# Performance work log

Hardware: AMD Instinct MI355X
Metric: run time of the kernel (lower is better)

The kernel has to match this reference:

```python
import jax, jax.numpy as jnp
import numpy as np

N, E, CIN, COUT = 50000, 800000, 64, 64
K_MAIN, K_SC = 5, 1
EPS = 1e-15      # PyG GMMConv sigma epsilon
BN_EPS = 1e-5    # BatchNorm epsilon


def gmm_conv(x, src, dst, pseudo, g, mu, sigma, root, bias):
    """PyG GMMConv with aggr='mean', root_weight=True, bias=True.
    x: [N,Cin], pseudo: [E,dim], g: [Cin,K*Cout], mu/sigma: [K,dim],
    root: [Cin,Cout], bias: [Cout]."""
    K = mu.shape[0]
    Cout = root.shape[1]
    n = x.shape[0]
    # Gaussian mixture weights per edge: [E,K]
    diff = pseudo[:, None, :] - mu[None, :, :]                     # [E,K,dim]
    gauss = jnp.exp((-0.5 * diff * diff / (EPS + sigma[None] ** 2)).sum(-1))
    # Project node features once at node level, then gather per edge
    xp = (x @ g).reshape(n, K, Cout)                               # [N,K,Cout]
    msg = jnp.einsum('ek,ekc->ec', gauss, xp[src])                 # [E,Cout]
    agg = jax.ops.segment_sum(msg, dst, num_segments=n)            # [N,Cout]
    deg = jax.ops.segment_sum(jnp.ones((src.shape[0],), x.dtype), dst,
                              num_segments=n)
    agg = agg / jnp.clip(deg, 1.0)[:, None]                        # mean aggr
    return agg + x @ root + bias


def batch_norm(x, gamma, beta):
    # SyncBatchNorm in training mode: batch stats over the node dimension
    m = x.mean(0)
    v = x.var(0)  # biased variance, as torch uses for normalization
    return (x - m) * jax.lax.rsqrt(v + BN_EPS) * gamma + beta


def _gmm_params(key, cin, cout, k):
    k1, k2, k3, k4 = jax.random.split(key, 4)
    scale = 1.0 / np.sqrt(cin)
    g = jax.random.normal(k1, (cin, k * cout), jnp.float32) * scale
    mu = jax.random.uniform(k2, (k, 1), jnp.float32)
    sigma = 1.0 + 0.1 * jax.random.uniform(k3, (k, 1), jnp.float32)
    root = jax.random.normal(k4, (cin, cout), jnp.float32) * scale
    bias = jnp.zeros((cout,), jnp.float32)
    return g, mu, sigma, root, bias


def setup_inputs() -> dict:
    key = jax.random.key(0)
    ks = jax.random.split(key, 8)
    x = jax.random.normal(ks[0], (N, CIN), jnp.float32)
    edge_index = jax.random.randint(ks[1], (2, E), 0, N, jnp.int64)
    edge_attr = jax.random.uniform(ks[2], (E, 1), jnp.float32)
    g1, mu1, sig1, root1, b1 = _gmm_params(ks[3], CIN, COUT, K_MAIN)
    g2, mu2, sig2, root2, b2 = _gmm_params(ks[4], COUT, COUT, K_MAIN)
    gs, mus, sigs, roots, bs = _gmm_params(ks[5], CIN, COUT, K_SC)
    ones = jnp.ones((COUT,), jnp.float32)
    zeros = jnp.zeros((COUT,), jnp.float32)
    return {
        'x': x, 'edge_index': edge_index, 'edge_attr': edge_attr,
        'g1': g1, 'mu1': mu1, 'sig1': sig1, 'root1': root1, 'b1': b1,
        'gam1': ones, 'bet1': zeros,
        'g2': g2, 'mu2': mu2, 'sig2': sig2, 'root2': root2, 'b2': b2,
        'gam2': ones, 'bet2': zeros,
        'gs': gs, 'mus': mus, 'sigs': sigs, 'roots': roots, 'bs': bs,
        'gams': ones, 'bets': zeros,
    }


def reference(x, edge_index, edge_attr,
              g1, mu1, sig1, root1, b1, gam1, bet1,
              g2, mu2, sig2, root2, b2, gam2, bet2,
              gs, mus, sigs, roots, bs, gams, bets):
    src, dst = edge_index[0], edge_index[1]
    h = gmm_conv(x, src, dst, edge_attr, g1, mu1, sig1, root1, b1)
    h = jax.nn.elu(batch_norm(h, gam1, bet1))
    h = gmm_conv(h, src, dst, edge_attr, g2, mu2, sig2, root2, b2)
    h = batch_norm(h, gam2, bet2)
    sc = gmm_conv(x, src, dst, edge_attr, gs, mus, sigs, roots, bs)
    sc = batch_norm(sc, gams, bets)
    return jax.nn.elu(h + sc)
```

## Files before the change

### kernel.cpp

```cpp
#include <hip/hip_runtime.h>
#include <hip/hip_bf16.h>


#define EPS_SIGMA 1e-15f
#define BN_EPS    1e-5f

typedef unsigned short ushortT;
typedef unsigned int uintT;
typedef __attribute__((ext_vector_type(8))) short bf16x8;
typedef __attribute__((ext_vector_type(4))) float f32x4;
typedef __attribute__((ext_vector_type(2))) float f32x2;

__device__ __forceinline__ ushortT f2bf(float f) {
  uintT b = __float_as_uint(f);
  b += 0x7FFFu + ((b >> 16) & 1u);
  return (ushortT)(b >> 16);
}
__device__ __forceinline__ float bf2f(ushortT u) {
  return __uint_as_float(((uintT)u) << 16);
}
__device__ __forceinline__ uintT pk2(float a, float b) {
  return (uintT)f2bf(a) | ((uintT)f2bf(b) << 16);
}

__global__ void prologue(const float* __restrict__ x, ushortT* __restrict__ x_bf,
                         int total, int* __restrict__ cnt, float* __restrict__ stats,
                         int n, const void* ei, int* flag) {
  int t = blockIdx.x * 256 + threadIdx.x;
  int idx = t * 4;
  if (idx + 3 < total) {
    float4 v = *(const float4*)&x[idx];
    ushortT o[4] = {f2bf(v.x), f2bf(v.y), f2bf(v.z), f2bf(v.w)};
    *(uint2*)&x_bf[idx] = *(const uint2*)o;
  }
  if (t < n) cnt[t] = 0;
  if (t < 12 * 64) stats[t] = 0.f;
  if (blockIdx.x == 0) {
    const int* p = (const int*)ei;
    __shared__ int bad;
    if (threadIdx.x == 0) bad = 0;
    __syncthreads();
    if (p[threadIdx.x * 2 + 1] != 0) atomicAdd(&bad, 1);
    __syncthreads();
    if (threadIdx.x == 0) *flag = (bad == 0);
  }
}

__device__ __forceinline__ int load_idx(const void* ei, size_t pos, int is64) {
  if (is64) return (int)((const long long*)ei)[pos];
  return ((const int*)ei)[pos];
}

__global__ void hist_kernel(const void* ei, int E, const int* flag, int* cnt,
                            int* __restrict__ pos) {
  int e = blockIdx.x * blockDim.x + threadIdx.x;
  if (e >= E) return;
  int d = load_idx(ei, (size_t)E + e, *flag);
  pos[e] = atomicAdd(&cnt[d], 1);
}

__global__ __launch_bounds__(256) void scan1(const int* __restrict__ cnt,
                                             int* __restrict__ row_ptr,
                                             int* __restrict__ partials, int n) {
  int tid = threadIdx.x;
  int base = blockIdx.x * 2048 + tid * 8;
  int v[8], pre[8];
  int run = 0;
#pragma unroll
  for (int j = 0; j < 8; ++j) {
    int idx = base + j;
    v[j] = (idx < n) ? cnt[idx] : 0;
    pre[j] = run;
    run += v[j];
  }
  __shared__ int sd[256];
  sd[tid] = run;
  __syncthreads();
  for (int off = 1; off < 256; off <<= 1) {
    int t = (tid >= off) ? sd[tid - off] : 0;
    __syncthreads();
    sd[tid] += t;
    __syncthreads();
  }
  int excl = sd[tid] - run;
#pragma unroll
  for (int j = 0; j < 8; ++j) {
    int idx = base + j;
    if (idx < n) row_ptr[idx] = excl + pre[j];
  }
  if (tid == 255) partials[blockIdx.x] = sd[255];
}

__global__ void scan2(int* partials, int nb, int* row_ptr, int n) {
  __shared__ int sd[256];
  int tid = threadIdx.x;
  int v = (tid < nb) ? partials[tid] : 0;
  sd[tid] = v;
  __syncthreads();
  for (int off = 1; off < 256; off <<= 1) {
    int t = (tid >= off) ? sd[tid - off] : 0;
    __syncthreads();
    sd[tid] += t;
    __syncthreads();
  }
  if (tid < nb) partials[tid] = sd[tid] - v;
  if (tid == nb - 1) row_ptr[n] = sd[tid];
}

__global__ void scan3(int* __restrict__ row_ptr, const int* __restrict__ partials, int n) {
  int i = blockIdx.x * 256 + threadIdx.x;
  if (i < n) row_ptr[i] += partials[i >> 11];
}

__global__ __launch_bounds__(256) void scatter_wgt(
    const void* ei, const float* __restrict__ ea, int E, const int* flag,
    const int* __restrict__ row_ptr, const int* __restrict__ pos,
    const float* __restrict__ mu1, const float* __restrict__ sig1,
    const float* __restrict__ mus, const float* __restrict__ sigs,
    const float* __restrict__ mu2, const float* __restrict__ sig2,
    uint4* __restrict__ wbuf1, uint4* __restrict__ wbuf2) {
  int e = blockIdx.x * 256 + threadIdx.x;
  if (e >= E) return;
  int is64 = *flag;
  int s = load_idx(ei, (size_t)e, is64);
  int d = load_idx(ei, (size_t)E + e, is64);
  int slot = row_ptr[d] + pos[e];
  float p = ea[e];
  float w1[6], w2[5];
#pragma unroll
  for (int k = 0; k < 5; ++k) {
    float sg = sig1[k], df = p - mu1[k];
    w1[k] = __expf(-0.5f / (EPS_SIGMA + sg * sg) * df * df);
  }
  {
    float sg = sigs[0], df = p - mus[0];
    w1[5] = __expf(-0.5f / (EPS_SIGMA + sg * sg) * df * df);
  }
#pragma unroll
  for (int k = 0; k < 5; ++k) {
    float sg = sig2[k], df = p - mu2[k];
    w2[k] = __expf(-0.5f / (EPS_SIGMA + sg * sg) * df * df);
  }
  wbuf1[slot] = make_uint4(pk2(w1[0], w1[1]), pk2(w1[2], w1[3]), pk2(w1[4], w1[5]), (uintT)s);
  wbuf2[slot] = make_uint4(pk2(w2[0], w2[1]), pk2(w2[2], w2[3]), pk2(w2[4], 0.f), (uintT)s);
}

template <int KT>
__device__ __forceinline__ void q_fma(f32x2* acc, uint4 r, uint2 xv) {
  f32x2 xlo, xhi;
  xlo.x = bf2f((ushortT)(xv.x & 0xffffu));
  xlo.y = bf2f((ushortT)(xv.x >> 16));
  xhi.x = bf2f((ushortT)(xv.y & 0xffffu));
  xhi.y = bf2f((ushortT)(xv.y >> 16));
  float w;
  f32x2 wv;
  w = bf2f((ushortT)(r.x & 0xffffu));
  wv.x = w; wv.y = w;
  acc[0] = __builtin_elementwise_fma(wv, xlo, acc[0]);
  acc[1] = __builtin_elementwise_fma(wv, xhi, acc[1]);
  if (KT > 1) {
    w = bf2f((ushortT)(r.x >> 16));
    wv.x = w; wv.y = w;
    acc[2] = __builtin_elementwise_fma(wv, xlo, acc[2]);
    acc[3] = __builtin_elementwise_fma(wv, xhi, acc[3]);
  }
  if (KT > 2) {
    w = bf2f((ushortT)(r.y & 0xffffu));
    wv.x = w; wv.y = w;
    acc[4] = __builtin_elementwise_fma(wv, xlo, acc[4]);
    acc[5] = __builtin_elementwise_fma(wv, xhi, acc[5]);
  }
  if (KT > 3) {
    w = bf2f((ushortT)(r.y >> 16));
    wv.x = w; wv.y = w;
    acc[6] = __builtin_elementwise_fma(wv, xlo, acc[6]);
    acc[7] = __builtin_elementwise_fma(wv, xhi, acc[7]);
  }
  if (KT > 4) {
    w = bf2f((ushortT)(r.z & 0xffffu));
    wv.x = w; wv.y = w;
    acc[8] = __builtin_elementwise_fma(wv, xlo, acc[8]);
    acc[9] = __builtin_elementwise_fma(wv, xhi, acc[9]);
  }
  if (KT > 5) {
    w = bf2f((ushortT)(r.z >> 16));
    wv.x = w; wv.y = w;
    acc[10] = __builtin_elementwise_fma(wv, xlo, acc[10]);
    acc[11] = __builtin_elementwise_fma(wv, xhi, acc[11]);
  }
}

template <int KT>
__global__ __launch_bounds__(256) void agg_pre(const ushortT* __restrict__ feat,
                                               const int* __restrict__ row_ptr,
                                               const uint4* __restrict__ wbuf,
                                               ushortT* __restrict__ out, int n, int ldo) {
  int node = blockIdx.x * 4 + (threadIdx.x >> 6);
  int lane = threadIdx.x & 63;
  int q = lane >> 4;
  int c4 = lane & 15;
  if (node >= n) return;
  int beg = row_ptr[node], end = row_ptr[node + 1];
  f32x2 acc[2 * KT];
#pragma unroll
  for (int k = 0; k < 2 * KT; ++k) acc[k] = (f32x2){0.f, 0.f};
  int i = beg;
  for (; i + 8 <= end; i += 8) {
    uint4 r0 = wbuf[i + q];
    uint4 r1 = wbuf[i + 4 + q];
    uint2 x0 = *(const uint2*)&feat[((size_t)r0.w << 6) + c4 * 4];
    uint2 x1 = *(const uint2*)&feat[((size_t)r1.w << 6) + c4 * 4];
    q_fma<KT>(acc, r0, x0);
    q_fma<KT>(acc, r1, x1);
  }
  for (; i + 4 <= end; i += 4) {
    uint4 r = wbuf[i + q];
    uint2 xv = *(const uint2*)&feat[((size_t)r.w << 6) + c4 * 4];
    q_fma<KT>(acc, r, xv);
  }
  int rem = end - i;
  if (q < rem) {
    uint4 r = wbuf[i + q];
    uint2 xv = *(const uint2*)&feat[((size_t)r.w << 6) + c4 * 4];
    q_fma<KT>(acc, r, xv);
  }
#pragma unroll
  for (int k = 0; k < 2 * KT; ++k) {
    acc[k].x += __shfl_xor(acc[k].x, 16);
    acc[k].y += __shfl_xor(acc[k].y, 16);
    acc[k].x += __shfl_xor(acc[k].x, 32);
    acc[k].y += __shfl_xor(acc[k].y, 32);
  }
  int degi = end - beg;
  float invdeg = 1.0f / (float)(degi > 1 ? degi : 1);
  if (lane < 16) {
    uintT* outu = (uintT*)out;
    size_t obase = ((size_t)node * ldo) >> 1;
#pragma unroll
    for (int k = 0; k < KT; ++k) {
      uint2 ov = make_uint2(pk2(acc[2 * k].x * invdeg, acc[2 * k].y * invdeg),
                            pk2(acc[2 * k + 1].x * invdeg, acc[2 * k + 1].y * invdeg));
      *(uint2*)&outu[obase + k * 32 + c4 * 2] = ov;
    }
  }
}

__device__ __forceinline__ void prep_one(const float* __restrict__ g,
                                         const float* __restrict__ root,
                                         ushortT* __restrict__ Bm, int K, int t) {
  int ks = t >> 8, rem = t & 255;
  int nt = rem >> 6, lane = rem & 63;
  int kbase = ks * 32 + (lane >> 4) * 8;
  int col = nt * 16 + (lane & 15);
  ushortT o[8];
#pragma unroll
  for (int j = 0; j < 8; ++j) {
    int r = kbase + j;
    float v;
    if (r < K * 64) {
      int k = r >> 6, i = r & 63;
      v = g[(size_t)i * (K * 64) + k * 64 + col];
    } else {
      v = root[(size_t)(r - K * 64) * 64 + col];
    }
    o[j] = f2bf(v);
  }
  *(uint4*)&Bm[(size_t)t * 8] = *(const uint4*)o;
}

__global__ void prep_all(const float* g1, const float* root1, ushortT* Bm1,
                         const float* g2, const float* root2, ushortT* Bm2,
                         const float* gs, const float* roots, ushortT* Bmsc) {
  int t = blockIdx.x * 256 + threadIdx.x;
  if (t < 12 * 256) prep_one(g1, root1, Bm1, 5, t);
  else if (t < 24 * 256) prep_one(g2, root2, Bm2, 5, t - 12 * 256);
  else if (t < 28 * 256) prep_one(gs, roots, Bmsc, 1, t - 24 * 256);
}

__device__ __forceinline__ void bn_epilogue(float cs[4], float cq[4], int wid, int lane,
                                            int tid, float red_s[4][64], float red_q[4][64],
                                            float* sums, float* sumsq) {
#pragma unroll
  for (int nt = 0; nt < 4; ++nt) {
    cs[nt] += __shfl_xor(cs[nt], 16);
    cs[nt] += __shfl_xor(cs[nt], 32);
    cq[nt] += __shfl_xor(cq[nt], 16);
    cq[nt] += __shfl_xor(cq[nt], 32);
  }
  if (lane < 16) {
#pragma unroll
    for (int nt = 0; nt < 4; ++nt) {
      red_s[wid][nt * 16 + lane] = cs[nt];
      red_q[wid][nt * 16 + lane] = cq[nt];
    }
  }
  __syncthreads();
  if (tid < 64) {
    float ts = red_s[0][tid] + red_s[1][tid] + red_s[2][tid] + red_s[3][tid];
    float tq = red_q[0][tid] + red_q[1][tid] + red_q[2][tid] + red_q[3][tid];
    atomicAdd(&sums[tid], ts);
    atomicAdd(&sumsq[tid], tq);
  }
  __syncthreads();
}

__global__ __launch_bounds__(256) void gemm_mfma(const ushortT* __restrict__ A1, int lda1,
                                                 int K1, const ushortT* __restrict__ A2,
                                                 const ushortT* __restrict__ Bm,
                                                 const float* __restrict__ bias,
                                                 ushortT* __restrict__ C, int M,
                                                 float* sums, float* sumsq) {
  __shared__ float red_s[4][64];
  __shared__ float red_q[4][64];
  int tid = threadIdx.x;
  int wid = tid >> 6, lane = tid & 63;
  int row16 = lane & 15, kg = lane >> 4;
  int rowbase = blockIdx.x * 64 + wid * 16;
  int arow = rowbase + row16;
  if (arow >= M) arow = M - 1;
  const ushortT* a1p = A1 + (size_t)arow * lda1 + kg * 8;
  const ushortT* a2p = A2 + (size_t)arow * 64 + kg * 8;
  int nks1 = K1 >> 5;
  int nks = (K1 + 64) >> 5;
  f32x4 acc[4];
#pragma unroll
  for (int nt = 0; nt < 4; ++nt) acc[nt] = (f32x4){0.f, 0.f, 0.f, 0.f};
  for (int ks = 0; ks < nks; ++ks) {
    const ushortT* ap = (ks < nks1) ? (a1p + ks * 32) : (a2p + (ks - nks1) * 32);
    bf16x8 af = *(const bf16x8*)ap;
#pragma unroll
    for (int nt = 0; nt < 4; ++nt) {
      bf16x8 bfr = *(const bf16x8*)(Bm + (size_t)ks * 2048 + nt * 512 + lane * 8);
      acc[nt] = __builtin_amdgcn_mfma_f32_16x16x32_bf16(af, bfr, acc[nt], 0, 0, 0);
    }
  }
  float bv[4];
#pragma unroll
  for (int nt = 0; nt < 4; ++nt) bv[nt] = bias[nt * 16 + row16];
  float cs[4] = {}, cq[4] = {};
#pragma unroll
  for (int r = 0; r < 4; ++r) {
    int orow = rowbase + kg * 4 + r;
    if (orow < M) {
#pragma unroll
      for (int nt = 0; nt < 4; ++nt) {
        float v = acc[nt][r] + bv[nt];
        C[(size_t)orow * 64 + nt * 16 + row16] = f2bf(v);
        cs[nt] += v;
        cq[nt] = fmaf(v, v, cq[nt]);
      }
    }
  }
  bn_epilogue(cs, cq, wid, lane, tid, red_s, red_q, sums, sumsq);
}

__global__ __launch_bounds__(256) void gemm_mfma_dual(
    const ushortT* __restrict__ Abuf, const ushortT* __restrict__ X,
    const ushortT* __restrict__ Bm1, const ushortT* __restrict__ Bmsc,
    const float* __restrict__ b1, const float* __restrict__ bs,
    ushortT* __restrict__ H, ushortT* __restrict__ S, int M,
    float* sumH, float* sqH, float* sumS, float* sqS) {
  __shared__ float red_s[4][64];
  __shared__ float red_q[4][64];
  int tid = threadIdx.x;
  int wid = tid >> 6, lane = tid & 63;
  int row16 = lane & 15, kg = lane >> 4;
  int rowbase = blockIdx.x * 64 + wid * 16;
  int arow = rowbase + row16;
  if (arow >= M) arow = M - 1;
  const ushortT* ab = Abuf + (size_t)arow * 384 + kg * 8;
  const ushortT* xb = X + (size_t)arow * 64 + kg * 8;
  f32x4 accH[4], accS[4];
#pragma unroll
  for (int nt = 0; nt < 4; ++nt) {
    accH[nt] = (f32x4){0.f, 0.f, 0.f, 0.f};
    accS[nt] = (f32x4){0.f, 0.f, 0.f, 0.f};
  }
  for (int ks = 0; ks < 10; ++ks) {
    bf16x8 af = *(const bf16x8*)(ab + ks * 32);
#pragma unroll
    for (int nt = 0; nt < 4; ++nt) {
      bf16x8 bfr = *(const bf16x8*)(Bm1 + (size_t)ks * 2048 + nt * 512 + lane * 8);
      accH[nt] = __builtin_amdgcn_mfma_f32_16x16x32_bf16(af, bfr, accH[nt], 0, 0, 0);
    }
  }
#pragma unroll
  for (int ks = 0; ks < 2; ++ks) {
    bf16x8 af = *(const bf16x8*)(ab + 320 + ks * 32);
#pragma unroll
    for (int nt = 0; nt < 4; ++nt) {
      bf16x8 bfr = *(const bf16x8*)(Bmsc + (size_t)ks * 2048 + nt * 512 + lane * 8);
      accS[nt] = __builtin_amdgcn_mfma_f32_16x16x32_bf16(af, bfr, accS[nt], 0, 0, 0);
    }
  }
#pragma unroll
  for (int ks = 0; ks < 2; ++ks) {
    bf16x8 af = *(const bf16x8*)(xb + ks * 32);
#pragma unroll
    for (int nt = 0; nt < 4; ++nt) {
      bf16x8 bfrH = *(const bf16x8*)(Bm1 + (size_t)(10 + ks) * 2048 + nt * 512 + lane * 8);
      accH[nt] = __builtin_amdgcn_mfma_f32_16x16x32_bf16(af, bfrH, accH[nt], 0, 0, 0);
      bf16x8 bfrS = *(const bf16x8*)(Bmsc + (size_t)(2 + ks) * 2048 + nt * 512 + lane * 8);
      accS[nt] = __builtin_amdgcn_mfma_f32_16x16x32_bf16(af, bfrS, accS[nt], 0, 0, 0);
    }
  }
  float bvH[4], bvS[4];
#pragma unroll
  for (int nt = 0; nt < 4; ++nt) {
    bvH[nt] = b1[nt * 16 + row16];
    bvS[nt] = bs[nt * 16 + row16];
  }
  float csH[4] = {}, cqH[4] = {}, csS[4] = {}, cqS[4] = {};
#pragma unroll
  for (int r = 0; r < 4; ++r) {
    int orow = rowbase + kg * 4 + r;
    if (orow < M) {
#pragma unroll
      for (int nt = 0; nt < 4; ++nt) {
        float vh = accH[nt][r] + bvH[nt];
        float vs = accS[nt][r] + bvS[nt];
        H[(size_t)orow * 64 + nt * 16 + row16] = f2bf(vh);
        S[(size_t)orow * 64 + nt * 16 + row16] = f2bf(vs);
        csH[nt] += vh;
        cqH[nt] = fmaf(vh, vh, cqH[nt]);
        csS[nt] += vs;
        cqS[nt] = fmaf(vs, vs, cqS[nt]);
      }
    }
  }
  bn_epilogue(csH, cqH, wid, lane, tid, red_s, red_q, sumH, sqH);
  bn_epilogue(csS, cqS, wid, lane, tid, red_s, red_q, sumS, sqS);
}

__global__ void norm_elu(const ushortT* __restrict__ Hbf, ushortT* __restrict__ h_bf,
                         const float* __restrict__ stats, const float* __restrict__ gam,
                         const float* __restrict__ bet, float inv_n, int total4) {
  __shared__ float sc_s[64], sh_s[64];
  int tid = threadIdx.x;
  if (tid < 64) {
    float m = stats[tid] * inv_n;
    float v = stats[64 + tid] * inv_n - m * m;
    float r = rsqrtf(v + BN_EPS);
    float s = r * gam[tid];
    sc_s[tid] = s;
    sh_s[tid] = bet[tid] - m * s;
  }
  __syncthreads();
  int t = blockIdx.x * 256 + tid;
  if (t >= total4) return;
  int idx = t * 4;
  int c = idx & 63;
  uint2 hv = *(const uint2*)&Hbf[idx];
  float v0 = bf2f((ushortT)(hv.x & 0xffffu)) * sc_s[c] + sh_s[c];
  float v1 = bf2f((ushortT)(hv.x >> 16)) * sc_s[c + 1] + sh_s[c + 1];
  float v2 = bf2f((ushortT)(hv.y & 0xffffu)) * sc_s[c + 2] + sh_s[c + 2];
  float v3 = bf2f((ushortT)(hv.y >> 16)) * sc_s[c + 3] + sh_s[c + 3];
  v0 = v0 > 0.f ? v0 : expm1f(v0);
  v1 = v1 > 0.f ? v1 : expm1f(v1);
  v2 = v2 > 0.f ? v2 : expm1f(v2);
  v3 = v3 > 0.f ? v3 : expm1f(v3);
  *(uint2*)&h_bf[idx] = make_uint2(pk2(v0, v1), pk2(v2, v3));
}

__global__ void final_kernel(const ushortT* __restrict__ h2, const ushortT* __restrict__ scb,
                             const float* __restrict__ stats,
                             const float* __restrict__ gam2, const float* __restrict__ bet2,
                             const float* __restrict__ gams, const float* __restrict__ bets,
                             float inv_n, float* __restrict__ out, int total4) {
  __shared__ float s2_s[64], t2_s[64], ss_s[64], ts_s[64];
  int tid = threadIdx.x;
  if (tid < 64) {
    float m = stats[2 * 64 + tid] * inv_n;
    float v = stats[3 * 64 + tid] * inv_n - m * m;
    float r = rsqrtf(v + BN_EPS);
    float s = r * gam2[tid];
    s2_s[tid] = s;
    t2_s[tid] = bet2[tid] - m * s;
  } else if (tid < 128) {
    int c = tid - 64;
    float m = stats[4 * 64 + c] * inv_n;
    float v = stats[5 * 64 + c] * inv_n - m * m;
    float r = rsqrtf(v + BN_EPS);
    float s = r * gams[c];
    ss_s[c] = s;
    ts_s[c] = bets[c] - m * s;
  }
  __syncthreads();
  int t = blockIdx.x * 256 + tid;
  if (t >= total4) return;
  int idx = t * 4;
  int c = idx & 63;
  uint2 hv = *(const uint2*)&h2[idx];
  uint2 sv = *(const uint2*)&scb[idx];
  float v0 = bf2f((ushortT)(hv.x & 0xffffu)) * s2_s[c] + t2_s[c] +
             bf2f((ushortT)(sv.x & 0xffffu)) * ss_s[c] + ts_s[c];
  float v1 = bf2f((ushortT)(hv.x >> 16)) * s2_s[c + 1] + t2_s[c + 1] +
             bf2f((ushortT)(sv.x >> 16)) * ss_s[c + 1] + ts_s[c + 1];
  float v2 = bf2f((ushortT)(hv.y & 0xffffu)) * s2_s[c + 2] + t2_s[c + 2] +
             bf2f((ushortT)(sv.y & 0xffffu)) * ss_s[c + 2] + ts_s[c + 2];
  float v3 = bf2f((ushortT)(hv.y >> 16)) * s2_s[c + 3] + t2_s[c + 3] +
             bf2f((ushortT)(sv.y >> 16)) * ss_s[c + 3] + ts_s[c + 3];
  float4 o;
  o.x = v0 > 0.f ? v0 : expm1f(v0);
  o.y = v1 > 0.f ? v1 : expm1f(v1);
  o.z = v2 > 0.f ? v2 : expm1f(v2);
  o.w = v3 > 0.f ? v3 : expm1f(v3);
  *(float4*)&out[idx] = o;
}

extern "C" void kernel_launch(void* const* d_in, const int* in_sizes, int n_in,
                              void* d_out, int out_size, void* d_ws, size_t ws_size,
                              hipStream_t stream) {
  const float* x    = (const float*)d_in[0];
  const void*  ei   = d_in[1];
  const float* ea   = (const float*)d_in[2];
  const float* g1   = (const float*)d_in[3];
  const float* mu1  = (const float*)d_in[4];
  const float* sig1 = (const float*)d_in[5];
  const float* root1= (const float*)d_in[6];
  const float* b1   = (const float*)d_in[7];
  const float* gam1 = (const float*)d_in[8];
  const float* bet1 = (const float*)d_in[9];
  const float* g2   = (const float*)d_in[10];
  const float* mu2  = (const float*)d_in[11];
  const float* sig2 = (const float*)d_in[12];
  const float* root2= (const float*)d_in[13];
  const float* b2   = (const float*)d_in[14];
  const float* gam2 = (const float*)d_in[15];
  const float* bet2 = (const float*)d_in[16];
  const float* gs   = (const float*)d_in[17];
  const float* mus  = (const float*)d_in[18];
  const float* sigs = (const float*)d_in[19];
  const float* roots= (const float*)d_in[20];
  const float* bs   = (const float*)d_in[21];
  const float* gams = (const float*)d_in[22];
  const float* bets = (const float*)d_in[23];

  int N = in_sizes[0] / 64;
  int E = in_sizes[1] / 2;

  char* w = (char*)d_ws;
  auto alloc = [&](size_t bytes) {
    char* p = w;
    w += (bytes + 255) & ~(size_t)255;
    return p;
  };
  int*     flag    = (int*)alloc(256);
  int*     cnt     = (int*)alloc((size_t)N * 4);
  int*     row_ptr = (int*)alloc((size_t)(N + 1) * 4);
  int*     partials= (int*)alloc(256 * 4);
  int*     pos     = (int*)alloc((size_t)E * 4);
  uint4*   wbuf1   = (uint4*)alloc((size_t)E * 16);
  uint4*   wbuf2   = (uint4*)alloc((size_t)E * 16);
  ushortT* Abuf    = (ushortT*)alloc((size_t)N * 384 * 2);
  ushortT* x_bf    = (ushortT*)alloc((size_t)N * 64 * 2);
  ushortT* h_bf    = (ushortT*)alloc((size_t)N * 64 * 2);
  ushortT* Hpre    = (ushortT*)alloc((size_t)N * 64 * 2);
  ushortT* h2b     = (ushortT*)alloc((size_t)N * 64 * 2);
  ushortT* scb     = (ushortT*)alloc((size_t)N * 64 * 2);
  ushortT* Bm1     = (ushortT*)alloc(12 * 2048 * 2);
  ushortT* Bm2     = (ushortT*)alloc(12 * 2048 * 2);
  ushortT* Bmsc    = (ushortT*)alloc(4 * 2048 * 2);
  float*   stats   = (float*)alloc(12 * 64 * 4);

  int eb = (E + 255) / 256;
  int nb1 = (N + 2047) / 2048;
  int total4 = (N * 64) / 4;
  int nb_e4 = (total4 + 255) / 256;
  float inv_n = 1.0f / (float)N;

  prologue<<<nb_e4, 256, 0, stream>>>(x, x_bf, N * 64, cnt, stats, N, ei, flag);
  prep_all<<<28, 256, 0, stream>>>(g1, root1, Bm1, g2, root2, Bm2, gs, roots, Bmsc);

  hist_kernel<<<eb, 256, 0, stream>>>(ei, E, flag, cnt, pos);
  scan1<<<nb1, 256, 0, stream>>>(cnt, row_ptr, partials, N);
  scan2<<<1, 256, 0, stream>>>(partials, nb1, row_ptr, N);
  scan3<<<(N + 255) / 256, 256, 0, stream>>>(row_ptr, partials, N);
  scatter_wgt<<<eb, 256, 0, stream>>>(ei, ea, E, flag, row_ptr, pos,
                                      mu1, sig1, mus, sigs, mu2, sig2, wbuf1, wbuf2);

  int mtiles = (N + 63) / 64;
  int nb_node = (N + 3) / 4;

  agg_pre<6><<<nb_node, 256, 0, stream>>>(x_bf, row_ptr, wbuf1, Abuf, N, 384);
  gemm_mfma_dual<<<mtiles, 256, 0, stream>>>(Abuf, x_bf, Bm1, Bmsc, b1, bs, Hpre, scb, N,
                                             stats + 0 * 64, stats + 1 * 64,
                                             stats + 4 * 64, stats + 5 * 64);
  norm_elu<<<nb_e4, 256, 0, stream>>>(Hpre, h_bf, stats, gam1, bet1, inv_n, total4);

  agg_pre<5><<<nb_node, 256, 0, stream>>>(h_bf, row_ptr, wbuf2, Abuf, N, 320);
  gemm_mfma<<<mtiles, 256, 0, stream>>>(Abuf, 320, 320, h_bf, Bm2, b2, h2b, N,
                                        stats + 2 * 64, stats + 3 * 64);

  final_kernel<<<nb_e4, 256, 0, stream>>>(h2b, scb, stats, gam2, bet2, gams, bets,
                                          inv_n, (float*)d_out, total4);
}
```

Before: 227.0 us.

## Assign one node per 16-lane quarter-wave in aggregation, dropping cross-lane reduction

Aggregation previously split each node's edges across four 16-lane groups of a wavefront and combined them with shuffle reductions. Each 16-lane quarter now owns a whole node and walks its edges serially, unrolled by four, so the shuffles and the lane<16 write-out restriction go away. This removes the reduction overhead and keeps all lanes writing output, at the cost of divergence between quarters when node degrees differ and a longer per-lane serial dependency chain.

```diff
diff --git a/kernel.cpp b/kernel.cpp
--- a/kernel.cpp
+++ b/kernel.cpp
@@ -195,45 +195,39 @@
                                                const int* __restrict__ row_ptr,
                                                const uint4* __restrict__ wbuf,
                                                ushortT* __restrict__ out, int n, int ldo) {
-  int node = blockIdx.x * 4 + (threadIdx.x >> 6);
   int lane = threadIdx.x & 63;
   int q = lane >> 4;
   int c4 = lane & 15;
-  if (node >= n) return;
-  int beg = row_ptr[node], end = row_ptr[node + 1];
+  int node = (blockIdx.x * 4 + (threadIdx.x >> 6)) * 4 + q;
+  bool act = node < n;
+  int beg = act ? row_ptr[node] : 0;
+  int end = act ? row_ptr[node + 1] : 0;
   f32x2 acc[2 * KT];
 #pragma unroll
   for (int k = 0; k < 2 * KT; ++k) acc[k] = (f32x2){0.f, 0.f};
   int i = beg;
-  for (; i + 8 <= end; i += 8) {
-    uint4 r0 = wbuf[i + q];
-    uint4 r1 = wbuf[i + 4 + q];
+  for (; i + 4 <= end; i += 4) {
+    uint4 r0 = wbuf[i + 0];
+    uint4 r1 = wbuf[i + 1];
+    uint4 r2 = wbuf[i + 2];
+    uint4 r3 = wbuf[i + 3];
     uint2 x0 = *(const uint2*)&feat[((size_t)r0.w << 6) + c4 * 4];
     uint2 x1 = *(const uint2*)&feat[((size_t)r1.w << 6) + c4 * 4];
+    uint2 x2 = *(const uint2*)&feat[((size_t)r2.w << 6) + c4 * 4];
+    uint2 x3 = *(const uint2*)&feat[((size_t)r3.w << 6) + c4 * 4];
     q_fma<KT>(acc, r0, x0);
     q_fma<KT>(acc, r1, x1);
-  }
-  for (; i + 4 <= end; i += 4) {
-    uint4 r = wbuf[i + q];
+    q_fma<KT>(acc, r2, x2);
+    q_fma<KT>(acc, r3, x3);
+  }
+  for (; i < end; ++i) {
+    uint4 r = wbuf[i];
     uint2 xv = *(const uint2*)&feat[((size_t)r.w << 6) + c4 * 4];
     q_fma<KT>(acc, r, xv);
   }
-  int rem = end - i;
-  if (q < rem) {
-    uint4 r = wbuf[i + q];
-    uint2 xv = *(const uint2*)&feat[((size_t)r.w << 6) + c4 * 4];
-    q_fma<KT>(acc, r, xv);
-  }
-#pragma unroll
-  for (int k = 0; k < 2 * KT; ++k) {
-    acc[k].x += __shfl_xor(acc[k].x, 16);
-    acc[k].y += __shfl_xor(acc[k].y, 16);
-    acc[k].x += __shfl_xor(acc[k].x, 32);
-    acc[k].y += __shfl_xor(acc[k].y, 32);
-  }
-  int degi = end - beg;
-  float invdeg = 1.0f / (float)(degi > 1 ? degi : 1);
-  if (lane < 16) {
+  if (act) {
+    int degi = end - beg;
+    float invdeg = 1.0f / (float)(degi > 1 ? degi : 1);
     uintT* outu = (uintT*)out;
     size_t obase = ((size_t)node * ldo) >> 1;
 #pragma unroll
@@ -580,15 +574,15 @@
                                       mu1, sig1, mus, sigs, mu2, sig2, wbuf1, wbuf2);
 
   int mtiles = (N + 63) / 64;
-  int nb_node = (N + 3) / 4;
-
-  agg_pre<6><<<nb_node, 256, 0, stream>>>(x_bf, row_ptr, wbuf1, Abuf, N, 384);
+  int nb_node16 = (N + 15) / 16;
+
+  agg_pre<6><<<nb_node16, 256, 0, stream>>>(x_bf, row_ptr, wbuf1, Abuf, N, 384);
   gemm_mfma_dual<<<mtiles, 256, 0, stream>>>(Abuf, x_bf, Bm1, Bmsc, b1, bs, Hpre, scb, N,
                                              stats + 0 * 64, stats + 1 * 64,
                                              stats + 4 * 64, stats + 5 * 64);
   norm_elu<<<nb_e4, 256, 0, stream>>>(Hpre, h_bf, stats, gam1, bet1, inv_n, total4);
 
-  agg_pre<5><<<nb_node, 256, 0, stream>>>(h_bf, row_ptr, wbuf2, Abuf, N, 320);
+  agg_pre<5><<<nb_node16, 256, 0, stream>>>(h_bf, row_ptr, wbuf2, Abuf, N, 320);
   gemm_mfma<<<mtiles, 256, 0, stream>>>(Abuf, 320, 320, h_bf, Bm2, b2, h2b, N,
                                         stats + 2 * 64, stats + 3 * 64);
 
```

New measurement: 211.2 us. 1.07x faster.
